# Performance work log

Hardware: AMD Instinct MI355X
Metric: run time of the kernel (lower is better)

Reference implementation:

```python
import jax, jax.numpy as jnp
import numpy as np

N_PROBLEMS = 50000
N_HIDDEN = 128
B, T = 32, 1024


def setup_inputs() -> dict:
    key = jax.random.key(0)
    k1, k2, k3, k4, k5 = jax.random.split(key, 5)
    y = jax.random.uniform(k1, (B, T), dtype=jnp.float32)
    problem_seq = jax.random.randint(k2, (B, T), 0, N_PROBLEMS)
    embd_weight = jax.random.normal(k3, (N_PROBLEMS, N_HIDDEN), dtype=jnp.float32)
    lam_w = jax.random.normal(k4, (N_HIDDEN, 1), dtype=jnp.float32) * (1.0 / np.sqrt(N_HIDDEN))
    lam_b = jax.random.normal(k5, (1,), dtype=jnp.float32) * 0.01
    return {"y": y, "problem_seq": problem_seq, "embd_weight": embd_weight,
            "lam_w": lam_w, "lam_b": lam_b}


def reference(y, problem_seq, embd_weight, lam_w, lam_b):
    # x: [B, t, h] embedded problem sequence
    x = embd_weight[problem_seq]
    # cosine-similarity matrix between timesteps: [B, t, t]
    mag = jnp.linalg.norm(embd_weight, axis=1)[problem_seq]      # [B, t]
    denom = mag[:, :, None] * mag[:, None, :]                    # [B, t, t]
    sim = jnp.einsum('bth,bsh->bts', x, x) / denom
    sim = (sim + 1.0) * 0.5
    t = sim.shape[1]
    # strictly-lower-triangular causal mask (tril with diagonal=-1)
    mask = jnp.tril(jnp.ones((t, t), dtype=sim.dtype), k=-1)
    sim = sim * mask
    # reversed cumsum over key axis (time-since accumulation)
    delta_t = jax.lax.cumsum(sim, axis=2, reverse=True)
    # per-query decay rate lambda: [B, t, 1]
    lam = jnp.exp(x @ lam_w + lam_b)
    weight = sim * jnp.exp(-lam * delta_t)
    weight_normed = weight / (weight.sum(axis=2, keepdims=True) + 1e-6)
    yhat = jnp.einsum('bs,bts->bt', y, weight_normed)
    return jnp.clip(yhat, 0.01, 0.99)
```

## Files before the change

kernel.cpp:

```cpp
#include <hip/hip_runtime.h>
#include <math.h>

#define BB 32
#define TT 1024
#define HH 128

typedef __attribute__((ext_vector_type(8))) short short8;
typedef __attribute__((ext_vector_type(4))) float floatx4;

__device__ __forceinline__ unsigned short f2bf(float f) {
    unsigned u = __float_as_uint(f);
    u += 0x7fffu + ((u >> 16) & 1u);
    return (unsigned short)(u >> 16);
}

__global__ __launch_bounds__(256)
void gather_norm(const int* __restrict__ seq,
                 const float* __restrict__ embd,
                 const float* __restrict__ lam_w,
                 const float* __restrict__ lam_b,
                 unsigned short* __restrict__ xbf,
                 float* __restrict__ lam) {
    int row  = blockIdx.x * 4 + (threadIdx.x >> 6);
    int lane = threadIdx.x & 63;
    int idx = seq[row];
    float2 v = ((const float2*)(embd + (size_t)idx * HH))[lane];
    float2 w = ((const float2*)lam_w)[lane];
    float ss = v.x * v.x + v.y * v.y;
    float dw = v.x * w.x + v.y * w.y;
    #pragma unroll
    for (int off = 32; off > 0; off >>= 1) {
        ss += __shfl_down(ss, off);
        dw += __shfl_down(dw, off);
    }
    ss = __shfl(ss, 0);
    dw = __shfl(dw, 0);
    float inv = 1.0f / sqrtf(ss);
    unsigned bx = f2bf(v.x * inv);
    unsigned by = f2bf(v.y * inv);
    ((unsigned*)xbf)[(size_t)row * 64 + lane] = bx | (by << 16);
    if (lane == 0) lam[row] = expf(dw + lam_b[0]);
}

__global__ __launch_bounds__(256)
void sim_kernel(const unsigned short* __restrict__ xbf,
                const float* __restrict__ lam,
                const float* __restrict__ y,
                float* __restrict__ out) {
    const int b    = blockIdx.x & 31;
    const int tt   = 63 - (blockIdx.x >> 5);
    const int tid  = threadIdx.x;
    const int wave = tid >> 6;
    const int lane = tid & 63;
    const int tl   = lane & 15;
    const int quad = lane >> 4;

    const int t = tt * 16 + tl;
    const size_t rowbase = (size_t)b * TT;
    const float lam_t = lam[rowbase + t];
    const float* yb = y + rowbase;

    __shared__ float Wc[4][16], Yc[4][16], Tc[4][16];

    short8 bq[4];
    const short8* qrow = (const short8*)(xbf + (rowbase + t) * HH);
    #pragma unroll
    for (int kk = 0; kk < 4; kk++) bq[kk] = qrow[kk * 4 + quad];

    const int n    = tt + 1;
    const int base = n >> 2, rem = n & 3;
    const int cnt   = base + (wave < rem ? 1 : 0);
    const int start = wave * base + (wave < rem ? wave : rem);
    const int end   = start + cnt;

    float wsum = 0.f, wy = 0.f, carry = 0.f;

    for (int st = end - 1; st >= start; --st) {
        const int s_base = st << 4;
        const short8* arow =
            (const short8*)(xbf + (rowbase + s_base + tl) * HH);
        floatx4 acc = {0.f, 0.f, 0.f, 0.f};
        #pragma unroll
        for (int kk = 0; kk < 4; kk++) {
            short8 af = arow[kk * 4 + quad];
            acc = __builtin_amdgcn_mfma_f32_16x16x32_bf16(af, bq[kk], acc, 0, 0, 0);
        }

        const int s0g = s_base + quad * 4;
        float v0 = (s0g + 0 < t) ? (acc[0] + 1.f) * 0.5f : 0.f;
        float v1 = (s0g + 1 < t) ? (acc[1] + 1.f) * 0.5f : 0.f;
        float v2 = (s0g + 2 < t) ? (acc[2] + 1.f) * 0.5f : 0.f;
        float v3 = (s0g + 3 < t) ? (acc[3] + 1.f) * 0.5f : 0.f;

        float suf3 = v3;
        float suf2 = v2 + suf3;
        float suf1 = v1 + suf2;
        float suf0 = v0 + suf1;
        float tot = suf0;

        float q0 = __shfl(tot, tl);
        float q1 = __shfl(tot, tl + 16);
        float q2 = __shfl(tot, tl + 32);
        float q3 = __shfl(tot, tl + 48);
        float higher = (quad < 1 ? q1 : 0.f) + (quad < 2 ? q2 : 0.f) +
                       (quad < 3 ? q3 : 0.f);
        float dbase = higher + carry;
        carry += (q0 + q1) + (q2 + q3);

        float4 yv = ((const float4*)(yb + s_base))[quad];
        float w0 = v0 * __expf(-lam_t * (suf0 + dbase));
        float w1 = v1 * __expf(-lam_t * (suf1 + dbase));
        float w2 = v2 * __expf(-lam_t * (suf2 + dbase));
        float w3 = v3 * __expf(-lam_t * (suf3 + dbase));
        wsum += (w0 + w1) + (w2 + w3);
        wy   += w0 * yv.x + w1 * yv.y + w2 * yv.z + w3 * yv.w;
    }

    float Wt = __shfl(wsum, tl) + __shfl(wsum, tl + 16) +
               __shfl(wsum, tl + 32) + __shfl(wsum, tl + 48);
    float Yt = __shfl(wy, tl) + __shfl(wy, tl + 16) +
               __shfl(wy, tl + 32) + __shfl(wy, tl + 48);
    float Tt = __shfl(carry, tl) + 0.f;
    if (quad == 0) {
        Wc[wave][tl] = Wt;
        Yc[wave][tl] = Yt;
        Tc[wave][tl] = Tt;
    }
    __syncthreads();

    if (tid < 16) {
        float lt = lam[rowbase + tt * 16 + tid];
        float A = 0.f, W = 0.f, Y = 0.f;
        #pragma unroll
        for (int c = 3; c >= 0; --c) {
            float sc = __expf(-lt * A);
            W += Wc[c][tid] * sc;
            Y += Yc[c][tid] * sc;
            A += Tc[c][tid];
        }
        float r = Y / (W + 1e-6f);
        out[rowbase + tt * 16 + tid] = fminf(fmaxf(r, 0.01f), 0.99f);
    }
}

extern "C" void kernel_launch(void* const* d_in, const int* in_sizes, int n_in,
                              void* d_out, int out_size, void* d_ws, size_t ws_size,
                              hipStream_t stream) {
    const float* y     = (const float*)d_in[0];
    const int*   seq   = (const int*)  d_in[1];
    const float* embd  = (const float*)d_in[2];
    const float* lam_w = (const float*)d_in[3];
    const float* lam_b = (const float*)d_in[4];
    float* out = (float*)d_out;

    unsigned short* xbf = (unsigned short*)d_ws;
    float* lam = (float*)(xbf + (size_t)BB * TT * HH);

    gather_norm<<<BB * TT / 4, 256, 0, stream>>>(seq, embd, lam_w, lam_b, xbf, lam);
    sim_kernel<<<BB * 64, 256, 0, stream>>>(xbf, lam, y, out);
}
```

Measured before the change: 121.4 us.

## Batch four key tiles per iteration in sim kernel and widen gather loads

The sim kernel now computes the MFMA similarity and per-tile totals for four key tiles at once, then resolves the reverse cumulative offsets for the group in closed form. This breaks the serial carry dependency between tile iterations, letting the loads and MFMAs of several tiles be in flight together. The gather kernel handles two rows per wave with float4 loads and xor-shuffle reductions. More live registers per thread may lower occupancy.

```diff
diff --git a/kernel.cpp b/kernel.cpp
--- a/kernel.cpp
+++ b/kernel.cpp
@@ -21,25 +21,26 @@
                  const float* __restrict__ lam_b,
                  unsigned short* __restrict__ xbf,
                  float* __restrict__ lam) {
-    int row  = blockIdx.x * 4 + (threadIdx.x >> 6);
-    int lane = threadIdx.x & 63;
-    int idx = seq[row];
-    float2 v = ((const float2*)(embd + (size_t)idx * HH))[lane];
-    float2 w = ((const float2*)lam_w)[lane];
-    float ss = v.x * v.x + v.y * v.y;
-    float dw = v.x * w.x + v.y * w.y;
+    const int lane = threadIdx.x & 63;
+    const int half = lane >> 5;
+    const int l32  = lane & 31;
+    const int row  = blockIdx.x * 8 + (threadIdx.x >> 6) * 2 + half;
+    const int idx  = seq[row];
+    float4 v = ((const float4*)(embd + (size_t)idx * HH))[l32];
+    float4 w = ((const float4*)lam_w)[l32];
+    float ss = v.x * v.x + v.y * v.y + v.z * v.z + v.w * v.w;
+    float dw = v.x * w.x + v.y * w.y + v.z * w.z + v.w * w.w;
     #pragma unroll
-    for (int off = 32; off > 0; off >>= 1) {
-        ss += __shfl_down(ss, off);
-        dw += __shfl_down(dw, off);
+    for (int off = 16; off > 0; off >>= 1) {
+        ss += __shfl_xor(ss, off);
+        dw += __shfl_xor(dw, off);
     }
-    ss = __shfl(ss, 0);
-    dw = __shfl(dw, 0);
     float inv = 1.0f / sqrtf(ss);
-    unsigned bx = f2bf(v.x * inv);
-    unsigned by = f2bf(v.y * inv);
-    ((unsigned*)xbf)[(size_t)row * 64 + lane] = bx | (by << 16);
-    if (lane == 0) lam[row] = expf(dw + lam_b[0]);
+    unsigned b0 = f2bf(v.x * inv), b1 = f2bf(v.y * inv);
+    unsigned b2 = f2bf(v.z * inv), b3 = f2bf(v.w * inv);
+    uint2 o; o.x = b0 | (b1 << 16); o.y = b2 | (b3 << 16);
+    ((uint2*)(xbf + (size_t)row * HH))[l32] = o;
+    if (l32 == 0) lam[row] = expf(dw + lam_b[0]);
 }
 
 __global__ __launch_bounds__(256)
@@ -71,60 +72,82 @@
     const int base = n >> 2, rem = n & 3;
     const int cnt   = base + (wave < rem ? 1 : 0);
     const int start = wave * base + (wave < rem ? wave : rem);
-    const int end   = start + cnt;
 
-    float wsum = 0.f, wy = 0.f, carry = 0.f;
+    float wsum = 0.f, wy = 0.f, run = 0.f;
 
-    for (int st = end - 1; st >= start; --st) {
-        const int s_base = st << 4;
-        const short8* arow =
-            (const short8*)(xbf + (rowbase + s_base + tl) * HH);
-        floatx4 acc = {0.f, 0.f, 0.f, 0.f};
+    const int nsb = (cnt + 3) >> 2;
+    for (int sb = nsb - 1; sb >= 0; --sb) {
+        float vv[4][4];
+        float tT[4], hq[4];
+
         #pragma unroll
-        for (int kk = 0; kk < 4; kk++) {
-            short8 af = arow[kk * 4 + quad];
-            acc = __builtin_amdgcn_mfma_f32_16x16x32_bf16(af, bq[kk], acc, 0, 0, 0);
+        for (int j = 0; j < 4; j++) {
+            const int i = sb * 4 + j;
+            float v0 = 0.f, v1 = 0.f, v2 = 0.f, v3 = 0.f;
+            if (i < cnt) {
+                const int s_base = (start + i) << 4;
+                const short8* arow =
+                    (const short8*)(xbf + (rowbase + s_base + tl) * HH);
+                floatx4 acc = {0.f, 0.f, 0.f, 0.f};
+                #pragma unroll
+                for (int kk = 0; kk < 4; kk++) {
+                    short8 af = arow[kk * 4 + quad];
+                    acc = __builtin_amdgcn_mfma_f32_16x16x32_bf16(af, bq[kk], acc, 0, 0, 0);
+                }
+                const int s0g = s_base + quad * 4;
+                v0 = (s0g + 0 < t) ? (acc[0] + 1.f) * 0.5f : 0.f;
+                v1 = (s0g + 1 < t) ? (acc[1] + 1.f) * 0.5f : 0.f;
+                v2 = (s0g + 2 < t) ? (acc[2] + 1.f) * 0.5f : 0.f;
+                v3 = (s0g + 3 < t) ? (acc[3] + 1.f) * 0.5f : 0.f;
+            }
+            vv[j][0] = v0; vv[j][1] = v1; vv[j][2] = v2; vv[j][3] = v3;
+            float ts = (v0 + v1) + (v2 + v3);
+            float q0 = __shfl(ts, tl);
+            float q1 = __shfl(ts, tl + 16);
+            float q2 = __shfl(ts, tl + 32);
+            float q3 = __shfl(ts, tl + 48);
+            tT[j] = (q0 + q1) + (q2 + q3);
+            hq[j] = (quad < 1 ? q1 : 0.f) + (quad < 2 ? q2 : 0.f) +
+                    (quad < 3 ? q3 : 0.f);
         }
 
-        const int s0g = s_base + quad * 4;
-        float v0 = (s0g + 0 < t) ? (acc[0] + 1.f) * 0.5f : 0.f;
-        float v1 = (s0g + 1 < t) ? (acc[1] + 1.f) * 0.5f : 0.f;
-        float v2 = (s0g + 2 < t) ? (acc[2] + 1.f) * 0.5f : 0.f;
-        float v3 = (s0g + 3 < t) ? (acc[3] + 1.f) * 0.5f : 0.f;
+        float d3 = hq[3] + run;
+        float d2 = hq[2] + tT[3] + run;
+        float d1 = hq[1] + (tT[2] + tT[3]) + run;
+        float d0 = hq[0] + (tT[1] + (tT[2] + tT[3])) + run;
+        run += (tT[0] + tT[1]) + (tT[2] + tT[3]);
+        float dbase[4] = {d0, d1, d2, d3};
 
-        float suf3 = v3;
-        float suf2 = v2 + suf3;
-        float suf1 = v1 + suf2;
-        float suf0 = v0 + suf1;
-        float tot = suf0;
-
-        float q0 = __shfl(tot, tl);
-        float q1 = __shfl(tot, tl + 16);
-        float q2 = __shfl(tot, tl + 32);
-        float q3 = __shfl(tot, tl + 48);
-        float higher = (quad < 1 ? q1 : 0.f) + (quad < 2 ? q2 : 0.f) +
-                       (quad < 3 ? q3 : 0.f);
-        float dbase = higher + carry;
-        carry += (q0 + q1) + (q2 + q3);
-
-        float4 yv = ((const float4*)(yb + s_base))[quad];
-        float w0 = v0 * __expf(-lam_t * (suf0 + dbase));
-        float w1 = v1 * __expf(-lam_t * (suf1 + dbase));
-        float w2 = v2 * __expf(-lam_t * (suf2 + dbase));
-        float w3 = v3 * __expf(-lam_t * (suf3 + dbase));
-        wsum += (w0 + w1) + (w2 + w3);
-        wy   += w0 * yv.x + w1 * yv.y + w2 * yv.z + w3 * yv.w;
+        #pragma unroll
+        for (int j = 0; j < 4; j++) {
+            const int i = sb * 4 + j;
+            if (i < cnt) {
+                const int s_base = (start + i) << 4;
+                float v0 = vv[j][0], v1 = vv[j][1], v2 = vv[j][2], v3 = vv[j][3];
+                float suf3 = v3;
+                float suf2 = v2 + suf3;
+                float suf1 = v1 + suf2;
+                float suf0 = v0 + suf1;
+                float db = dbase[j];
+                float4 yv = ((const float4*)(yb + s_base))[quad];
+                float w0 = v0 * __expf(-lam_t * (suf0 + db));
+                float w1 = v1 * __expf(-lam_t * (suf1 + db));
+                float w2 = v2 * __expf(-lam_t * (suf2 + db));
+                float w3 = v3 * __expf(-lam_t * (suf3 + db));
+                wsum += (w0 + w1) + (w2 + w3);
+                wy   += w0 * yv.x + w1 * yv.y + w2 * yv.z + w3 * yv.w;
+            }
+        }
     }
 
     float Wt = __shfl(wsum, tl) + __shfl(wsum, tl + 16) +
                __shfl(wsum, tl + 32) + __shfl(wsum, tl + 48);
     float Yt = __shfl(wy, tl) + __shfl(wy, tl + 16) +
                __shfl(wy, tl + 32) + __shfl(wy, tl + 48);
-    float Tt = __shfl(carry, tl) + 0.f;
     if (quad == 0) {
         Wc[wave][tl] = Wt;
         Yc[wave][tl] = Yt;
-        Tc[wave][tl] = Tt;
+        Tc[wave][tl] = run;
     }
     __syncthreads();
 
@@ -156,6 +179,6 @@
     unsigned short* xbf = (unsigned short*)d_ws;
     float* lam = (float*)(xbf + (size_t)BB * TT * HH);
 
-    gather_norm<<<BB * TT / 4, 256, 0, stream>>>(seq, embd, lam_w, lam_b, xbf, lam);
+    gather_norm<<<BB * TT / 8, 256, 0, stream>>>(seq, embd, lam_w, lam_b, xbf, lam);
     sim_kernel<<<BB * 64, 256, 0, stream>>>(xbf, lam, y, out);
 }
```

New measurement: 117.4 us. 1.03x faster.
